# Optimization experiments

Hardware: AMD Instinct MI355X
Metric: run time of the kernel (lower is better)

## Reference

```python
import jax, jax.numpy as jnp
import numpy as np

N = 50000          # nodes
E = 500000         # edges (avg degree 10)
WIDTH = 128        # node feature width
HID = 128          # width * scale, scale=1 -> 2 heads of 64
HEAD = 64          # head_dim (module-level constant)
EMB = WIDTH // 2   # edge-embed width = 64
RES = 1.0
BOND = (5, 6, 2, 17)  # bond_size vocabularies


def setup_inputs() -> dict:
    key = jax.random.key(0)
    ks = jax.random.split(key, 24)
    w = lambda k, s: (jax.random.normal(k, s, jnp.float32) * 0.02)
    inp = {
        "x": jax.random.normal(ks[0], (N, WIDTH), jnp.float32),
        "edge_index": jax.random.randint(ks[1], (2, E), 0, N),
        "edge_attr": jax.random.randint(ks[2], (E, 4), 0, 3),
        # pre: Linear(width, width)
        "pre_w": w(ks[3], (WIDTH, WIDTH)), "pre_b": jnp.zeros((WIDTH,), jnp.float32),
        # msg[0..3]: Linear(width, hidden)
        "msg0_w": w(ks[4], (WIDTH, HID)), "msg0_b": jnp.zeros((HID,), jnp.float32),
        "msg1_w": w(ks[5], (WIDTH, HID)), "msg1_b": jnp.zeros((HID,), jnp.float32),
        "msg2_w": w(ks[6], (WIDTH, HID)), "msg2_b": jnp.zeros((HID,), jnp.float32),
        "msg3_w": w(ks[7], (WIDTH, HID)), "msg3_b": jnp.zeros((HID,), jnp.float32),
        # remix[0..2]: Linear(width//2, hidden)
        "remix0_w": w(ks[8], (EMB, HID)), "remix0_b": jnp.zeros((HID,), jnp.float32),
        "remix1_w": w(ks[9], (EMB, HID)), "remix1_b": jnp.zeros((HID,), jnp.float32),
        "remix2_w": w(ks[10], (EMB, HID)), "remix2_b": jnp.zeros((HID,), jnp.float32),
        # post: Linear(hidden, width)
        "post_w": w(ks[11], (HID, WIDTH)), "post_b": jnp.zeros((WIDTH,), jnp.float32),
        # EmbedBlock tables (bond_size + 1 rows each); tables 1..3 have padding_idx=0
        "emb0": w(ks[12], (BOND[0] + 1, EMB)),
        "emb1": w(ks[13], (BOND[1] + 1, EMB)).at[0].set(0.0),
        "emb2": w(ks[14], (BOND[2] + 1, EMB)).at[0].set(0.0),
        "emb3": w(ks[15], (BOND[3] + 1, EMB)).at[0].set(0.0),
        "einit": jnp.zeros((4,), jnp.float32),          # EmbedBlock.init0
        "init0": jnp.zeros((4,), jnp.float32),          # ConvBlock.init0 (hop*2+2)
    }
    return inp


def _gelu(v):
    return jax.nn.gelu(v, approximate=False)


def _ln(v):
    m = jnp.mean(v, axis=-1, keepdims=True)
    var = jnp.mean(jnp.square(v - m), axis=-1, keepdims=True)
    return (v - m) / jnp.sqrt(var + 1e-5)


def reference(x, edge_index, edge_attr, pre_w, pre_b, msg0_w, msg0_b,
              msg1_w, msg1_b, msg2_w, msg2_b, msg3_w, msg3_b,
              remix0_w, remix0_b, remix1_w, remix1_b, remix2_w, remix2_b,
              post_w, post_b, emb0, emb1, emb2, emb3, einit, init0):
    n = x.shape[0]
    e = edge_index.shape[1]
    xx = _ln(x @ pre_w + pre_b)  # pre: Linear + LayerNorm(no affine)
    # EmbedBlock: weighted sum of per-column embeddings, xw = exp(a)/sqrt(sum exp(a))
    xw = jnp.exp(einit) / jnp.sqrt(jnp.sum(jnp.exp(einit)))
    ee = (emb0[edge_attr[:, 0]] * xw[0] + emb1[edge_attr[:, 1]] * xw[1]
          + emb2[edge_attr[:, 2]] * xw[2] + emb3[edge_attr[:, 3]] * xw[3])  # [E, 64]
    src, dst = edge_index[0], edge_index[1]  # source_to_target: j=src, i=dst
    x_j = xx[src]
    x_i = xx[dst]
    scale_e = jnp.exp(init0[-2])
    scale_v = jnp.exp(init0[-1])
    q = x_i @ msg1_w + msg1_b + (ee @ remix0_w + remix0_b) * scale_e  # [E, HID]
    k = x_j @ msg2_w + msg2_b + (ee @ remix1_w + remix1_b) * scale_e
    v = _gelu(x_j @ msg3_w + msg3_b + (ee @ remix2_w + remix2_b) * scale_v)
    # per-head attention score, head_dim = 64
    att = jnp.sum((q * k).reshape(e, -1, HEAD), axis=-1, keepdims=True) / np.sqrt(HEAD)
    att = jnp.exp(att * init0[0] + init0[1])  # edge_type=0, hop=1
    msg = (v.reshape(e, -1, HEAD) * att).reshape(e, -1)  # [E, HID]
    agg = jax.ops.segment_sum(msg, dst, num_segments=n)  # scatter-add to targets
    xx = _gelu(xx @ msg0_w + msg0_b) + agg
    out = xx @ post_w + post_b
    return x + out * RES
```

## Files before the change

### kernel.cpp

```cpp
#include <hip/hip_runtime.h>
#include <cstdint>

#define WIDTH 128
#define NCOMBO 2268
#define XSL 136

typedef short bf16x8 __attribute__((ext_vector_type(8)));
typedef float f32x4  __attribute__((ext_vector_type(4)));

__device__ __forceinline__ float gelu_fast(float v) {
    float e = __expf(v * __builtin_fmaf(v * v, 0.0713548f, 1.5957691f));
    return v - v * __builtin_amdgcn_rcpf(e + 1.0f);
}
__device__ __forceinline__ short f2b(float f) {
    unsigned u = __float_as_uint(f);
    unsigned r = (u + 0x7FFFu + ((u >> 16) & 1u)) >> 16;
    return (short)r;
}
__device__ __forceinline__ float b2f(unsigned short s) {
    return __uint_as_float(((unsigned)s) << 16);
}
__device__ __forceinline__ float b2f_lo(unsigned u) { return __uint_as_float(u << 16); }
__device__ __forceinline__ float b2f_hi(unsigned u) { return __uint_as_float(u & 0xFFFF0000u); }
__device__ __forceinline__ unsigned pack2(float lo, float hi) {
    return (unsigned)(unsigned short)f2b(lo) | ((unsigned)(unsigned short)f2b(hi) << 16);
}

__global__ void k_prep(const float* __restrict__ einit, const float* __restrict__ init0,
                       const float* __restrict__ emb0, const float* __restrict__ emb1,
                       const float* __restrict__ emb2, const float* __restrict__ emb3,
                       const float* __restrict__ r0w, const float* __restrict__ r0b,
                       const float* __restrict__ r1w, const float* __restrict__ r1b,
                       const float* __restrict__ r2w, const float* __restrict__ r2b,
                       const float* __restrict__ pw0, const float* __restrict__ pw1,
                       const float* __restrict__ pw2, const float* __restrict__ pw3,
                       const float* __restrict__ pw4, const float* __restrict__ pw5,
                       short* __restrict__ o0, short* __restrict__ o1,
                       short* __restrict__ o2, short* __restrict__ o3,
                       short* __restrict__ o4, short* __restrict__ o5,
                       float* __restrict__ U, float* __restrict__ scal,
                       int* __restrict__ counts, int n) {
    int tid = blockIdx.x * blockDim.x + threadIdx.x;
    if (tid == 0) { scal[0] = init0[0]; scal[1] = init0[1]; }
    const int TOTW = 6 * 16384;
    const int TOTU = 3 * 34 * WIDTH;
    if (tid < TOTW) {
        int which = tid >> 14;
        int r = tid & 16383;
        int k = r >> 7, nn = r & 127;
        const float* w = (which == 0) ? pw0 : (which == 1) ? pw1 : (which == 2) ? pw2
                       : (which == 3) ? pw3 : (which == 4) ? pw4 : pw5;
        short* o = (which == 0) ? o0 : (which == 1) ? o1 : (which == 2) ? o2
                 : (which == 3) ? o3 : (which == 4) ? o4 : o5;
        o[nn * 128 + k] = f2b(w[k * 128 + nn]);
    } else if (tid < TOTW + TOTU) {
        int idx = tid - TOTW;
        float e0 = expf(einit[0]), e1 = expf(einit[1]), e2 = expf(einit[2]), e3 = expf(einit[3]);
        float inv = 1.0f / sqrtf(e0 + e1 + e2 + e3);
        float xw[4] = {e0 * inv, e1 * inv, e2 * inv, e3 * inv};
        float se = expf(init0[2]);
        float sv = expf(init0[3]);
        int r   = idx / (34 * WIDTH);
        int rem = idx - r * (34 * WIDTH);
        int g   = rem / WIDTH;
        int j   = rem - g * WIDTH;
        int cc, base;
        if (g >= 16)      { cc = 3; base = 16; }
        else if (g >= 13) { cc = 2; base = 13; }
        else if (g >= 6)  { cc = 1; base = 6; }
        else              { cc = 0; base = 0; }
        int i = g - base;
        const float* em = (cc == 0) ? emb0 : (cc == 1) ? emb1 : (cc == 2) ? emb2 : emb3;
        const float* w  = (r == 0) ? r0w : (r == 1) ? r1w : r2w;
        const float* rb = (r == 0) ? r0b : (r == 1) ? r1b : r2b;
        float s = (r == 2) ? sv : se;
        float acc = 0.0f;
        const float* erow = em + i * 64;
        for (int d = 0; d < 64; ++d) acc += erow[d] * w[d * WIDTH + j];
        float val = s * xw[cc] * acc;
        if (cc == 0) val += s * rb[j];
        U[idx] = val;
    } else if (tid < TOTW + TOTU + n) {
        counts[tid - TOTW - TOTU] = 0;
    }
}

__global__ void k_prepc(const float* __restrict__ U, const float* __restrict__ init0,
                        float* __restrict__ Uc) {
    int bi = blockIdx.x;
    int r  = bi / NCOMBO;
    if (r < 2 && init0[0] == 0.0f) return;
    int cb = bi - r * NCOMBO;
    int a  = cb / 378;
    int rm = cb - a * 378;
    int b  = rm / 54;
    rm -= b * 54;
    int c  = rm / 18;
    int d  = rm - c * 18;
    int j  = threadIdx.x;
    const float* Ur = U + r * 34 * WIDTH;
    Uc[(size_t)bi * WIDTH + j] = Ur[a * WIDTH + j] + Ur[(6 + b) * WIDTH + j]
                               + Ur[(13 + c) * WIDTH + j] + Ur[(16 + d) * WIDTH + j];
}

__global__ void k_hist(const int* __restrict__ edge_index, int* __restrict__ counts,
                       int* __restrict__ rank, int E) {
    int e = blockIdx.x * blockDim.x + threadIdx.x;
    if (e >= E) return;
    rank[e] = atomicAdd(&counts[edge_index[E + e]], 1);
}

__global__ void k_scan1(const int* __restrict__ counts, int* __restrict__ lscan,
                        int* __restrict__ partials, int n) {
    __shared__ int s[256];
    int t = threadIdx.x;
    int i = blockIdx.x * 256 + t;
    int v = (i < n) ? counts[i] : 0;
    s[t] = v;
    __syncthreads();
    for (int d = 1; d < 256; d <<= 1) {
        int u = (t >= d) ? s[t - d] : 0;
        __syncthreads();
        s[t] += u;
        __syncthreads();
    }
    if (i < n) lscan[i] = s[t];
    if (t == 255) partials[blockIdx.x] = s[255];
}

__global__ void k_scan2(int* __restrict__ partials, int nb,
                        int* __restrict__ offsets, int n) {
    __shared__ int s[1024];
    int t = threadIdx.x;
    int v = (t < nb) ? partials[t] : 0;
    s[t] = v;
    __syncthreads();
    for (int d = 1; d < 1024; d <<= 1) {
        int u = (t >= d) ? s[t - d] : 0;
        __syncthreads();
        s[t] += u;
        __syncthreads();
    }
    if (t < nb) partials[t] = s[t] - v;
    if (t == 1023) offsets[n] = s[1023];
}

__global__ void k_scan3(const int* __restrict__ counts, const int* __restrict__ lscan,
                        const int* __restrict__ partials, int* __restrict__ offsets, int n) {
    int i = blockIdx.x * 256 + threadIdx.x;
    if (i >= n) return;
    offsets[i] = partials[blockIdx.x] + lscan[i] - counts[i];
}

__global__ void k_scatter(const int* __restrict__ edge_index, const int* __restrict__ edge_attr,
                          const int* __restrict__ offsets, const int* __restrict__ rank,
                          unsigned* __restrict__ s_pk, int E) {
    int e = blockIdx.x * blockDim.x + threadIdx.x;
    if (e >= E) return;
    int src = edge_index[e];
    int dst = edge_index[E + e];
    int4 at = ((const int4*)edge_attr)[e];
    int combo = ((at.x * 7 + at.y) * 3 + at.z) * 18 + at.w;
    s_pk[offsets[dst] + rank[e]] = (unsigned)src | ((unsigned)combo << 17);
}

__global__ void __launch_bounds__(256, 2) k_gemm12(
        const float* __restrict__ x,
        const short* __restrict__ preT, const float* __restrict__ pre_b,
        const short* __restrict__ w0T, const float* __restrict__ b0,
        const short* __restrict__ w1T, const float* __restrict__ b1,
        const short* __restrict__ w2T, const float* __restrict__ b2,
        const short* __restrict__ w3T, const float* __restrict__ b3,
        const float* __restrict__ scal,
        short* __restrict__ Gb, float* __restrict__ A,
        short* __restrict__ Bb, short* __restrict__ Cb, int n) {
    __shared__ short xs[64 * XSL];
    int w    = threadIdx.x >> 6;
    int lane = threadIdx.x & 63;
    int quad = lane >> 4, l16 = lane & 15;
    int m0   = blockIdx.x * 64;

    bf16x8 Bg[2][4], Bc[2][4];
#pragma unroll
    for (int tt = 0; tt < 2; ++tt)
#pragma unroll
        for (int kc = 0; kc < 4; ++kc) {
            int row = (2 * w + tt) * 16 + l16;
            Bg[tt][kc] = *(const bf16x8*)(w0T + row * 128 + kc * 32 + quad * 8);
            Bc[tt][kc] = *(const bf16x8*)(w3T + row * 128 + kc * 32 + quad * 8);
        }

    {
        int mrow = m0 + w * 16;
        int mA = min(mrow + l16, n - 1);
        bf16x8 a[4];
#pragma unroll
        for (int kc = 0; kc < 4; ++kc) {
            const float* px = x + (size_t)mA * WIDTH + kc * 32 + quad * 8;
            float4 f0 = *(const float4*)(px);
            float4 f1 = *(const float4*)(px + 4);
            bf16x8 av;
            av[0] = f2b(f0.x); av[1] = f2b(f0.y); av[2] = f2b(f0.z); av[3] = f2b(f0.w);
            av[4] = f2b(f1.x); av[5] = f2b(f1.y); av[6] = f2b(f1.z); av[7] = f2b(f1.w);
            a[kc] = av;
        }
        f32x4 acc[8];
#pragma unroll
        for (int t = 0; t < 8; ++t) acc[t] = (f32x4){0.f, 0.f, 0.f, 0.f};
#pragma unroll
        for (int kc = 0; kc < 4; ++kc) {
#pragma unroll
            for (int t = 0; t < 8; ++t) {
                bf16x8 b = *(const bf16x8*)(preT + (t * 16 + l16) * 128 + kc * 32 + quad * 8);
                acc[t] = __builtin_amdgcn_mfma_f32_16x16x32_bf16(a[kc], b, acc[t], 0, 0, 0);
            }
        }
#pragma unroll
        for (int t = 0; t < 8; ++t) {
            float bv = pre_b[t * 16 + l16];
#pragma unroll
            for (int r = 0; r < 4; ++r) acc[t][r] += bv;
        }
#pragma unroll
        for (int r = 0; r < 4; ++r) {
            float s = 0.f, s2 = 0.f;
#pragma unroll
            for (int t = 0; t < 8; ++t) { float v = acc[t][r]; s += v; s2 += v * v; }
            s  += __shfl_xor(s, 1);  s2 += __shfl_xor(s2, 1);
            s  += __shfl_xor(s, 2);  s2 += __shfl_xor(s2, 2);
            s  += __shfl_xor(s, 4);  s2 += __shfl_xor(s2, 4);
            s  += __shfl_xor(s, 8);  s2 += __shfl_xor(s2, 8);
            float m   = s * (1.0f / WIDTH);
            float var = s2 * (1.0f / WIDTH) - m * m;
            float rs  = rsqrtf(var + 1e-5f);
#pragma unroll
            for (int t = 0; t < 8; ++t) acc[t][r] = (acc[t][r] - m) * rs;
        }
        int rowb = w * 16 + quad * 4;
#pragma unroll
        for (int t = 0; t < 8; ++t)
#pragma unroll
            for (int r = 0; r < 4; ++r)
                xs[(rowb + r) * XSL + t * 16 + l16] = f2b(acc[t][r]);
    }
    __syncthreads();

    bf16x8 a2[4][4];
#pragma unroll
    for (int i = 0; i < 4; ++i)
#pragma unroll
        for (int kc = 0; kc < 4; ++kc)
            a2[i][kc] = *(const bf16x8*)(&xs[(i * 16 + l16) * XSL + kc * 32 + quad * 8]);

    {
        f32x4 accG[4][2], accC[4][2];
#pragma unroll
        for (int i = 0; i < 4; ++i)
#pragma unroll
            for (int tt = 0; tt < 2; ++tt) {
                accG[i][tt] = (f32x4){0.f,0.f,0.f,0.f};
                accC[i][tt] = (f32x4){0.f,0.f,0.f,0.f};
            }
#pragma unroll
        for (int kc = 0; kc < 4; ++kc)
#pragma unroll
            for (int i = 0; i < 4; ++i)
#pragma unroll
                for (int tt = 0; tt < 2; ++tt) {
                    accG[i][tt] = __builtin_amdgcn_mfma_f32_16x16x32_bf16(a2[i][kc], Bg[tt][kc], accG[i][tt], 0, 0, 0);
                    accC[i][tt] = __builtin_amdgcn_mfma_f32_16x16x32_bf16(a2[i][kc], Bc[tt][kc], accC[i][tt], 0, 0, 0);
                }
#pragma unroll
        for (int tt = 0; tt < 2; ++tt) {
            int col = (2 * w + tt) * 16 + l16;
            float bg = b0[col];
            float bc = b3[col];
#pragma unroll
            for (int i = 0; i < 4; ++i)
#pragma unroll
                for (int r = 0; r < 4; ++r) {
                    int row = m0 + i * 16 + quad * 4 + r;
                    if (row < n) {
                        size_t idx = (size_t)row * WIDTH + col;
                        Gb[idx] = f2b(gelu_fast(accG[i][tt][r] + bg));
                        Cb[idx] = f2b(accC[i][tt][r] + bc);
                    }
                }
        }
    }
    if (scal[0] != 0.0f) {
        bf16x8 Ba[2][4], Bbf[2][4];
#pragma unroll
        for (int tt = 0; tt < 2; ++tt)
#pragma unroll
            for (int kc = 0; kc < 4; ++kc) {
                int row = (2 * w + tt) * 16 + l16;
                Ba[tt][kc]  = *(const bf16x8*)(w1T + row * 128 + kc * 32 + quad * 8);
                Bbf[tt][kc] = *(const bf16x8*)(w2T + row * 128 + kc * 32 + quad * 8);
            }
        f32x4 accA[4][2], accB[4][2];
#pragma unroll
        for (int i = 0; i < 4; ++i)
#pragma unroll
            for (int tt = 0; tt < 2; ++tt) {
                accA[i][tt] = (f32x4){0.f,0.f,0.f,0.f};
                accB[i][tt] = (f32x4){0.f,0.f,0.f,0.f};
            }
#pragma unroll
        for (int kc = 0; kc < 4; ++kc)
#pragma unroll
            for (int i = 0; i < 4; ++i)
#pragma unroll
                for (int tt = 0; tt < 2; ++tt) {
                    accA[i][tt] = __builtin_amdgcn_mfma_f32_16x16x32_bf16(a2[i][kc], Ba[tt][kc],  accA[i][tt], 0, 0, 0);
                    accB[i][tt] = __builtin_amdgcn_mfma_f32_16x16x32_bf16(a2[i][kc], Bbf[tt][kc], accB[i][tt], 0, 0, 0);
                }
#pragma unroll
        for (int tt = 0; tt < 2; ++tt) {
            int col = (2 * w + tt) * 16 + l16;
            float ba = b1[col];
            float bb = b2[col];
#pragma unroll
            for (int i = 0; i < 4; ++i)
#pragma unroll
                for (int r = 0; r < 4; ++r) {
                    int row = m0 + i * 16 + quad * 4 + r;
                    if (row < n) {
                        size_t idx = (size_t)row * WIDTH + col;
                        A[idx]  = accA[i][tt][r] + ba;
                        Bb[idx] = f2b(accB[i][tt][r] + bb);
                    }
                }
        }
    }
}

__global__ void __launch_bounds__(256)
k_agg(const int* __restrict__ offsets, const unsigned* __restrict__ s_pk,
      const float* __restrict__ A, const short* __restrict__ Bb,
      const short* __restrict__ Cb, const float* __restrict__ Uc,
      const float* __restrict__ scal, const short* __restrict__ Gb,
      short* __restrict__ hb, int n) {
    int wid = threadIdx.x >> 6;
    int L   = threadIdx.x & 63;
    int node = blockIdx.x * 4 + wid;
    if (node >= n) return;
    int start = offsets[node];
    int end   = offsets[node + 1];

    const unsigned* Cb32 = (const unsigned*)Cb;
    const unsigned* Bb32 = (const unsigned*)Bb;
    const float2* U0c2 = (const float2*)(Uc);
    const float2* U1c2 = (const float2*)(Uc + (size_t)NCOMBO * WIDTH);
    const float2* U2c2 = (const float2*)(Uc + 2 * (size_t)NCOMBO * WIDTH);

    float i0 = scal[0], i1 = scal[1];
    float acc0 = 0.0f, acc1 = 0.0f;

    if (i0 == 0.0f) {
        int p = start;
        for (; p + 2 <= end; p += 2) {
            unsigned pk0 = s_pk[p], pk1 = s_pk[p + 1];
            unsigned sA = pk0 & 0x1FFFFu, cA = pk0 >> 17;
            unsigned sB = pk1 & 0x1FFFFu, cB = pk1 >> 17;
            unsigned cc0 = Cb32[sA * 64 + L];
            float2   uu0 = U2c2[cA * 64 + L];
            unsigned cc1 = Cb32[sB * 64 + L];
            float2   uu1 = U2c2[cB * 64 + L];
            acc0 += gelu_fast(b2f_lo(cc0) + uu0.x);
            acc1 += gelu_fast(b2f_hi(cc0) + uu0.y);
            acc0 += gelu_fast(b2f_lo(cc1) + uu1.x);
            acc1 += gelu_fast(b2f_hi(cc1) + uu1.y);
        }
        if (p < end) {
            unsigned pk0 = s_pk[p];
            unsigned sA = pk0 & 0x1FFFFu, cA = pk0 >> 17;
            unsigned cc0 = Cb32[sA * 64 + L];
            float2   uu0 = U2c2[cA * 64 + L];
            acc0 += gelu_fast(b2f_lo(cc0) + uu0.x);
            acc1 += gelu_fast(b2f_hi(cc0) + uu0.y);
        }
        float s = __expf(i1);
        acc0 *= s; acc1 *= s;
    } else {
        float2 av = *(const float2*)(A + (size_t)node * WIDTH + 2 * L);
        for (int p = start; p < end; ++p) {
            unsigned pk = s_pk[p];
            unsigned sA = pk & 0x1FFFFu, cA = pk >> 17;
            float2 u0 = U0c2[cA * 64 + L];
            float2 u1 = U1c2[cA * 64 + L];
            float2 u2 = U2c2[cA * 64 + L];
            unsigned bb = Bb32[sA * 64 + L];
            unsigned cc = Cb32[sA * 64 + L];
            float q0 = av.x + u0.x, q1 = av.y + u0.y;
            float k0 = b2f_lo(bb) + u1.x, k1 = b2f_hi(bb) + u1.y;
            float v0 = gelu_fast(b2f_lo(cc) + u2.x);
            float v1 = gelu_fast(b2f_hi(cc) + u2.y);
            float s = q0 * k0 + q1 * k1;
            s += __shfl_xor(s, 1);
            s += __shfl_xor(s, 2);
            s += __shfl_xor(s, 4);
            s += __shfl_xor(s, 8);
            s += __shfl_xor(s, 16);
            float att = __expf(s * 0.125f * i0 + i1);
            acc0 += v0 * att;
            acc1 += v1 * att;
        }
    }
    unsigned g = ((const unsigned*)Gb)[(size_t)node * 64 + L];
    ((unsigned*)hb)[(size_t)node * 64 + L] = pack2(b2f_lo(g) + acc0, b2f_hi(g) + acc1);
}

__global__ void __launch_bounds__(256, 2) k_post(
        const float* __restrict__ x, const short* __restrict__ hb,
        const short* __restrict__ postT, const float* __restrict__ post_b,
        float* __restrict__ out, int n) {
    int w    = threadIdx.x >> 6;
    int lane = threadIdx.x & 63;
    int quad = lane >> 4, l16 = lane & 15;
    int m0   = blockIdx.x * 64;

    bf16x8 Bp[2][4];
#pragma unroll
    for (int tt = 0; tt < 2; ++tt)
#pragma unroll
        for (int kc = 0; kc < 4; ++kc) {
            int row = (2 * w + tt) * 16 + l16;
            Bp[tt][kc] = *(const bf16x8*)(postT + row * 128 + kc * 32 + quad * 8);
        }

    bf16x8 a[4][4];
#pragma unroll
    for (int i = 0; i < 4; ++i) {
        int mA = min(m0 + i * 16 + l16, n - 1);
#pragma unroll
        for (int kc = 0; kc < 4; ++kc)
            a[i][kc] = *(const bf16x8*)(hb + (size_t)mA * WIDTH + kc * 32 + quad * 8);
    }

    f32x4 acc[4][2];
#pragma unroll
    for (int i = 0; i < 4; ++i)
#pragma unroll
        for (int tt = 0; tt < 2; ++tt) acc[i][tt] = (f32x4){0.f,0.f,0.f,0.f};
#pragma unroll
    for (int kc = 0; kc < 4; ++kc)
#pragma unroll
        for (int i = 0; i < 4; ++i)
#pragma unroll
            for (int tt = 0; tt < 2; ++tt)
                acc[i][tt] = __builtin_amdgcn_mfma_f32_16x16x32_bf16(a[i][kc], Bp[tt][kc], acc[i][tt], 0, 0, 0);

#pragma unroll
    for (int tt = 0; tt < 2; ++tt) {
        int col = (2 * w + tt) * 16 + l16;
        float bv = post_b[col];
#pragma unroll
        for (int i = 0; i < 4; ++i)
#pragma unroll
            for (int r = 0; r < 4; ++r) {
                int row = m0 + i * 16 + quad * 4 + r;
                if (row < n) {
                    size_t idx = (size_t)row * WIDTH + col;
                    out[idx] = x[idx] + acc[i][tt][r] + bv;
                }
            }
    }
}

extern "C" void kernel_launch(void* const* d_in, const int* in_sizes, int n_in,
                              void* d_out, int out_size, void* d_ws, size_t ws_size,
                              hipStream_t stream) {
    const float* x      = (const float*)d_in[0];
    const int*   eidx   = (const int*)d_in[1];
    const int*   eattr  = (const int*)d_in[2];
    const float* pre_w  = (const float*)d_in[3];
    const float* pre_b  = (const float*)d_in[4];
    const float* msg0_w = (const float*)d_in[5];
    const float* msg0_b = (const float*)d_in[6];
    const float* msg1_w = (const float*)d_in[7];
    const float* msg1_b = (const float*)d_in[8];
    const float* msg2_w = (const float*)d_in[9];
    const float* msg2_b = (const float*)d_in[10];
    const float* msg3_w = (const float*)d_in[11];
    const float* msg3_b = (const float*)d_in[12];
    const float* r0w    = (const float*)d_in[13];
    const float* r0b    = (const float*)d_in[14];
    const float* r1w    = (const float*)d_in[15];
    const float* r1b    = (const float*)d_in[16];
    const float* r2w    = (const float*)d_in[17];
    const float* r2b    = (const float*)d_in[18];
    const float* post_w = (const float*)d_in[19];
    const float* post_b = (const float*)d_in[20];
    const float* emb0   = (const float*)d_in[21];
    const float* emb1   = (const float*)d_in[22];
    const float* emb2   = (const float*)d_in[23];
    const float* emb3   = (const float*)d_in[24];
    const float* einit  = (const float*)d_in[25];
    const float* init0  = (const float*)d_in[26];

    int n = in_sizes[0] / WIDTH;
    int E = in_sizes[2] / 4;
    size_t NW = (size_t)n * WIDTH;

    float* ws   = (float*)d_ws;
    float* A    = ws;
    float* U    = ws + NW;
    float* Uc   = U + 3 * 34 * WIDTH;
    float* scal = Uc + 3 * (size_t)NCOMBO * WIDTH;
    short* sw   = (short*)(scal + 2);
    short* preT  = sw;
    short* w0T   = sw + 16384;
    short* w1T   = sw + 2 * 16384;
    short* w2T   = sw + 3 * 16384;
    short* w3T   = sw + 4 * 16384;
    short* postT = sw + 5 * 16384;
    short* Bb    = sw + 6 * 16384;
    short* Cb    = Bb + NW;
    short* Gb    = Cb + NW;
    short* hb    = Gb + NW;
    int*      ib       = (int*)(hb + NW);
    int*      offsets  = ib;
    int*      counts   = offsets + (n + 1);
    int*      lscan    = counts + n;
    int*      partials = lscan + n;
    int*      rank     = partials + 1024;
    unsigned* s_pk     = (unsigned*)(rank + E);

    int prep_total = 6 * 16384 + 3 * 34 * WIDTH + n;
    k_prep<<<(prep_total + 255) / 256, 256, 0, stream>>>(
        einit, init0, emb0, emb1, emb2, emb3,
        r0w, r0b, r1w, r1b, r2w, r2b,
        pre_w, msg0_w, msg1_w, msg2_w, msg3_w, post_w,
        preT, w0T, w1T, w2T, w3T, postT, U, scal, counts, n);
    k_prepc<<<3 * NCOMBO, 128, 0, stream>>>(U, init0, Uc);

    int eb = (E + 255) / 256;
    k_hist<<<eb, 256, 0, stream>>>(eidx, counts, rank, E);
    int sb = (n + 255) / 256;
    k_scan1<<<sb, 256, 0, stream>>>(counts, lscan, partials, n);
    k_scan2<<<1, 1024, 0, stream>>>(partials, sb, offsets, n);
    k_scan3<<<sb, 256, 0, stream>>>(counts, lscan, partials, offsets, n);
    k_scatter<<<eb, 256, 0, stream>>>(eidx, eattr, offsets, rank, s_pk, E);

    int gb = (n + 63) / 64;
    k_gemm12<<<gb, 256, 0, stream>>>(x, preT, pre_b, w0T, msg0_b, w1T, msg1_b,
                                     w2T, msg2_b, w3T, msg3_b, scal, Gb, A, Bb, Cb, n);
    k_agg<<<(n + 3) / 4, 256, 0, stream>>>(offsets, s_pk, A, Bb, Cb, Uc, scal, Gb, hb, n);
    k_post<<<gb, 256, 0, stream>>>(x, hb, postT, post_b, (float*)d_out, n);
}
```

Before: 280.3 us.

## Pre-swizzle weights into MFMA fragment order and stage GEMM I/O through LDS

Weights are now stored in the exact per-lane MFMA fragment order, so each wave's B-operand loads become contiguous 16-byte reads. In k_gemm12 and k_post, the x/hb input tiles are loaded cooperatively with coalesced vector loads into LDS, and the Gb/Cb and out tiles are written back through LDS as full-row vector stores. This replaces strided per-element global accesses. The cost is more shared memory per block, which may lower occupancy, and extra __syncthreads barriers.

```diff
diff --git a/kernel.cpp b/kernel.cpp
--- a/kernel.cpp
+++ b/kernel.cpp
@@ -4,6 +4,7 @@
 #define WIDTH 128
 #define NCOMBO 2268
 #define XSL 136
+#define OSL 132
 
 typedef short bf16x8 __attribute__((ext_vector_type(8)));
 typedef float f32x4  __attribute__((ext_vector_type(4)));
@@ -16,9 +17,6 @@
     unsigned u = __float_as_uint(f);
     unsigned r = (u + 0x7FFFu + ((u >> 16) & 1u)) >> 16;
     return (short)r;
-}
-__device__ __forceinline__ float b2f(unsigned short s) {
-    return __uint_as_float(((unsigned)s) << 16);
 }
 __device__ __forceinline__ float b2f_lo(unsigned u) { return __uint_as_float(u << 16); }
 __device__ __forceinline__ float b2f_hi(unsigned u) { return __uint_as_float(u & 0xFFFF0000u); }
@@ -47,12 +45,17 @@
     if (tid < TOTW) {
         int which = tid >> 14;
         int r = tid & 16383;
-        int k = r >> 7, nn = r & 127;
+        int t    = r >> 11;
+        int kc   = (r >> 9) & 3;
+        int lane = (r >> 3) & 63;
+        int j    = r & 7;
+        int k  = kc * 32 + ((lane >> 4) << 3) + j;
+        int nn = (t << 4) + (lane & 15);
         const float* w = (which == 0) ? pw0 : (which == 1) ? pw1 : (which == 2) ? pw2
                        : (which == 3) ? pw3 : (which == 4) ? pw4 : pw5;
         short* o = (which == 0) ? o0 : (which == 1) ? o1 : (which == 2) ? o2
                  : (which == 3) ? o3 : (which == 4) ? o4 : o5;
-        o[nn * 128 + k] = f2b(w[k * 128 + nn]);
+        o[r] = f2b(w[k * 128 + nn]);
     } else if (tid < TOTW + TOTU) {
         int idx = tid - TOTW;
         float e0 = expf(einit[0]), e1 = expf(einit[1]), e2 = expf(einit[2]), e3 = expf(einit[3]);
@@ -166,17 +169,19 @@
 
 __global__ void __launch_bounds__(256, 2) k_gemm12(
         const float* __restrict__ x,
-        const short* __restrict__ preT, const float* __restrict__ pre_b,
-        const short* __restrict__ w0T, const float* __restrict__ b0,
-        const short* __restrict__ w1T, const float* __restrict__ b1,
-        const short* __restrict__ w2T, const float* __restrict__ b2,
-        const short* __restrict__ w3T, const float* __restrict__ b3,
+        const short* __restrict__ preF, const float* __restrict__ pre_b,
+        const short* __restrict__ w0F, const float* __restrict__ b0,
+        const short* __restrict__ w1F, const float* __restrict__ b1,
+        const short* __restrict__ w2F, const float* __restrict__ b2,
+        const short* __restrict__ w3F, const float* __restrict__ b3,
         const float* __restrict__ scal,
         short* __restrict__ Gb, float* __restrict__ A,
         short* __restrict__ Bb, short* __restrict__ Cb, int n) {
-    __shared__ short xs[64 * XSL];
-    int w    = threadIdx.x >> 6;
-    int lane = threadIdx.x & 63;
+    __shared__ short xs_raw[64 * XSL];
+    __shared__ short xs_xx[64 * XSL];
+    int tid  = threadIdx.x;
+    int w    = tid >> 6;
+    int lane = tid & 63;
     int quad = lane >> 4, l16 = lane & 15;
     int m0   = blockIdx.x * 64;
 
@@ -185,36 +190,39 @@
     for (int tt = 0; tt < 2; ++tt)
 #pragma unroll
         for (int kc = 0; kc < 4; ++kc) {
-            int row = (2 * w + tt) * 16 + l16;
-            Bg[tt][kc] = *(const bf16x8*)(w0T + row * 128 + kc * 32 + quad * 8);
-            Bc[tt][kc] = *(const bf16x8*)(w3T + row * 128 + kc * 32 + quad * 8);
-        }
+            int fo = (((2 * w + tt) * 4 + kc) * 64 + lane) * 8;
+            Bg[tt][kc] = *(const bf16x8*)(w0F + fo);
+            Bc[tt][kc] = *(const bf16x8*)(w3F + fo);
+        }
+
+#pragma unroll
+    for (int it = 0; it < 8; ++it) {
+        int fi  = it * 256 + tid;
+        int row = fi >> 5, c4 = fi & 31;
+        int gr  = min(m0 + row, n - 1);
+        float4 v = ((const float4*)x)[(size_t)gr * 32 + c4];
+        uint2 p;
+        p.x = pack2(v.x, v.y);
+        p.y = pack2(v.z, v.w);
+        *(uint2*)(&xs_raw[row * XSL + c4 * 4]) = p;
+    }
+    __syncthreads();
 
     {
-        int mrow = m0 + w * 16;
-        int mA = min(mrow + l16, n - 1);
         bf16x8 a[4];
 #pragma unroll
-        for (int kc = 0; kc < 4; ++kc) {
-            const float* px = x + (size_t)mA * WIDTH + kc * 32 + quad * 8;
-            float4 f0 = *(const float4*)(px);
-            float4 f1 = *(const float4*)(px + 4);
-            bf16x8 av;
-            av[0] = f2b(f0.x); av[1] = f2b(f0.y); av[2] = f2b(f0.z); av[3] = f2b(f0.w);
-            av[4] = f2b(f1.x); av[5] = f2b(f1.y); av[6] = f2b(f1.z); av[7] = f2b(f1.w);
-            a[kc] = av;
-        }
+        for (int kc = 0; kc < 4; ++kc)
+            a[kc] = *(const bf16x8*)(&xs_raw[(w * 16 + l16) * XSL + kc * 32 + quad * 8]);
         f32x4 acc[8];
 #pragma unroll
         for (int t = 0; t < 8; ++t) acc[t] = (f32x4){0.f, 0.f, 0.f, 0.f};
 #pragma unroll
-        for (int kc = 0; kc < 4; ++kc) {
+        for (int kc = 0; kc < 4; ++kc)
 #pragma unroll
             for (int t = 0; t < 8; ++t) {
-                bf16x8 b = *(const bf16x8*)(preT + (t * 16 + l16) * 128 + kc * 32 + quad * 8);
+                bf16x8 b = *(const bf16x8*)(preF + ((t * 4 + kc) * 64 + lane) * 8);
                 acc[t] = __builtin_amdgcn_mfma_f32_16x16x32_bf16(a[kc], b, acc[t], 0, 0, 0);
             }
-        }
 #pragma unroll
         for (int t = 0; t < 8; ++t) {
             float bv = pre_b[t * 16 + l16];
@@ -241,7 +249,7 @@
         for (int t = 0; t < 8; ++t)
 #pragma unroll
             for (int r = 0; r < 4; ++r)
-                xs[(rowb + r) * XSL + t * 16 + l16] = f2b(acc[t][r]);
+                xs_xx[(rowb + r) * XSL + t * 16 + l16] = f2b(acc[t][r]);
     }
     __syncthreads();
 
@@ -250,7 +258,8 @@
     for (int i = 0; i < 4; ++i)
 #pragma unroll
         for (int kc = 0; kc < 4; ++kc)
-            a2[i][kc] = *(const bf16x8*)(&xs[(i * 16 + l16) * XSL + kc * 32 + quad * 8]);
+            a2[i][kc] = *(const bf16x8*)(&xs_xx[(i * 16 + l16) * XSL + kc * 32 + quad * 8]);
+    __syncthreads();
 
     {
         f32x4 accG[4][2], accC[4][2];
@@ -279,24 +288,33 @@
             for (int i = 0; i < 4; ++i)
 #pragma unroll
                 for (int r = 0; r < 4; ++r) {
-                    int row = m0 + i * 16 + quad * 4 + r;
-                    if (row < n) {
-                        size_t idx = (size_t)row * WIDTH + col;
-                        Gb[idx] = f2b(gelu_fast(accG[i][tt][r] + bg));
-                        Cb[idx] = f2b(accC[i][tt][r] + bc);
-                    }
+                    int row = i * 16 + quad * 4 + r;
+                    xs_raw[row * XSL + col] = f2b(gelu_fast(accG[i][tt][r] + bg));
+                    xs_xx[row * XSL + col]  = f2b(accC[i][tt][r] + bc);
                 }
         }
     }
+    __syncthreads();
+
+#pragma unroll
+    for (int it = 0; it < 4; ++it) {
+        int si  = it * 256 + tid;
+        int row = si >> 4, c8 = si & 15;
+        if (m0 + row < n) {
+            *(bf16x8*)(Gb + (size_t)(m0 + row) * WIDTH + c8 * 8) = *(const bf16x8*)(&xs_raw[row * XSL + c8 * 8]);
+            *(bf16x8*)(Cb + (size_t)(m0 + row) * WIDTH + c8 * 8) = *(const bf16x8*)(&xs_xx[row * XSL + c8 * 8]);
+        }
+    }
+
     if (scal[0] != 0.0f) {
         bf16x8 Ba[2][4], Bbf[2][4];
 #pragma unroll
         for (int tt = 0; tt < 2; ++tt)
 #pragma unroll
             for (int kc = 0; kc < 4; ++kc) {
-                int row = (2 * w + tt) * 16 + l16;
-                Ba[tt][kc]  = *(const bf16x8*)(w1T + row * 128 + kc * 32 + quad * 8);
-                Bbf[tt][kc] = *(const bf16x8*)(w2T + row * 128 + kc * 32 + quad * 8);
+                int fo = (((2 * w + tt) * 4 + kc) * 64 + lane) * 8;
+                Ba[tt][kc]  = *(const bf16x8*)(w1F + fo);
+                Bbf[tt][kc] = *(const bf16x8*)(w2F + fo);
             }
         f32x4 accA[4][2], accB[4][2];
 #pragma unroll
@@ -413,10 +431,13 @@
 
 __global__ void __launch_bounds__(256, 2) k_post(
         const float* __restrict__ x, const short* __restrict__ hb,
-        const short* __restrict__ postT, const float* __restrict__ post_b,
+        const short* __restrict__ postF, const float* __restrict__ post_b,
         float* __restrict__ out, int n) {
-    int w    = threadIdx.x >> 6;
-    int lane = threadIdx.x & 63;
+    __shared__ short hs[64 * XSL];
+    __shared__ float os[64 * OSL];
+    int tid  = threadIdx.x;
+    int w    = tid >> 6;
+    int lane = tid & 63;
     int quad = lane >> 4, l16 = lane & 15;
     int m0   = blockIdx.x * 64;
 
@@ -424,19 +445,24 @@
 #pragma unroll
     for (int tt = 0; tt < 2; ++tt)
 #pragma unroll
-        for (int kc = 0; kc < 4; ++kc) {
-            int row = (2 * w + tt) * 16 + l16;
-            Bp[tt][kc] = *(const bf16x8*)(postT + row * 128 + kc * 32 + quad * 8);
-        }
+        for (int kc = 0; kc < 4; ++kc)
+            Bp[tt][kc] = *(const bf16x8*)(postF + (((2 * w + tt) * 4 + kc) * 64 + lane) * 8);
+
+#pragma unroll
+    for (int it = 0; it < 4; ++it) {
+        int si  = it * 256 + tid;
+        int row = si >> 4, c8 = si & 15;
+        int gr  = min(m0 + row, n - 1);
+        *(bf16x8*)(&hs[row * XSL + c8 * 8]) = *(const bf16x8*)(hb + (size_t)gr * WIDTH + c8 * 8);
+    }
+    __syncthreads();
 
     bf16x8 a[4][4];
 #pragma unroll
-    for (int i = 0; i < 4; ++i) {
-        int mA = min(m0 + i * 16 + l16, n - 1);
-#pragma unroll
-        for (int kc = 0; kc < 4; ++kc)
-            a[i][kc] = *(const bf16x8*)(hb + (size_t)mA * WIDTH + kc * 32 + quad * 8);
-    }
+    for (int i = 0; i < 4; ++i)
+#pragma unroll
+        for (int kc = 0; kc < 4; ++kc)
+            a[i][kc] = *(const bf16x8*)(&hs[(i * 16 + l16) * XSL + kc * 32 + quad * 8]);
 
     f32x4 acc[4][2];
 #pragma unroll
@@ -458,13 +484,21 @@
 #pragma unroll
         for (int i = 0; i < 4; ++i)
 #pragma unroll
-            for (int r = 0; r < 4; ++r) {
-                int row = m0 + i * 16 + quad * 4 + r;
-                if (row < n) {
-                    size_t idx = (size_t)row * WIDTH + col;
-                    out[idx] = x[idx] + acc[i][tt][r] + bv;
-                }
-            }
+            for (int r = 0; r < 4; ++r)
+                os[(i * 16 + quad * 4 + r) * OSL + col] = acc[i][tt][r] + bv;
+    }
+    __syncthreads();
+
+#pragma unroll
+    for (int it = 0; it < 8; ++it) {
+        int fi  = it * 256 + tid;
+        int row = fi >> 5, c4 = fi & 31;
+        if (m0 + row < n) {
+            float4 xv = ((const float4*)x)[(size_t)(m0 + row) * 32 + c4];
+            float4 av = *(const float4*)(&os[row * OSL + c4 * 4]);
+            float4 ov = {xv.x + av.x, xv.y + av.y, xv.z + av.z, xv.w + av.w};
+            ((float4*)out)[(size_t)(m0 + row) * 32 + c4] = ov;
+        }
     }
 }
 
@@ -509,12 +543,12 @@
     float* Uc   = U + 3 * 34 * WIDTH;
     float* scal = Uc + 3 * (size_t)NCOMBO * WIDTH;
     short* sw   = (short*)(scal + 2);
-    short* preT  = sw;
-    short* w0T   = sw + 16384;
-    short* w1T   = sw + 2 * 16384;
-    short* w2T   = sw + 3 * 16384;
-    short* w3T   = sw + 4 * 16384;
-    short* postT = sw + 5 * 16384;
+    short* preF  = sw;
+    short* w0F   = sw + 16384;
+    short* w1F   = sw + 2 * 16384;
+    short* w2F   = sw + 3 * 16384;
+    short* w3F   = sw + 4 * 16384;
+    short* postF = sw + 5 * 16384;
     short* Bb    = sw + 6 * 16384;
     short* Cb    = Bb + NW;
     short* Gb    = Cb + NW;
@@ -532,7 +566,7 @@
         einit, init0, emb0, emb1, emb2, emb3,
         r0w, r0b, r1w, r1b, r2w, r2b,
         pre_w, msg0_w, msg1_w, msg2_w, msg3_w, post_w,
-        preT, w0T, w1T, w2T, w3T, postT, U, scal, counts, n);
+        preF, w0F, w1F, w2F, w3F, postF, U, scal, counts, n);
     k_prepc<<<3 * NCOMBO, 128, 0, stream>>>(U, init0, Uc);
 
     int eb = (E + 255) / 256;
@@ -544,8 +578,8 @@
     k_scatter<<<eb, 256, 0, stream>>>(eidx, eattr, offsets, rank, s_pk, E);
 
     int gb = (n + 63) / 64;
-    k_gemm12<<<gb, 256, 0, stream>>>(x, preT, pre_b, w0T, msg0_b, w1T, msg1_b,
-                                     w2T, msg2_b, w3T, msg3_b, scal, Gb, A, Bb, Cb, n);
+    k_gemm12<<<gb, 256, 0, stream>>>(x, preF, pre_b, w0F, msg0_b, w1F, msg1_b,
+                                     w2F, msg2_b, w3F, msg3_b, scal, Gb, A, Bb, Cb, n);
     k_agg<<<(n + 3) / 4, 256, 0, stream>>>(offsets, s_pk, A, Bb, Cb, Uc, scal, Gb, hb, n);
-    k_post<<<gb, 256, 0, stream>>>(x, hb, postT, post_b, (float*)d_out, n);
-}
+    k_post<<<gb, 256, 0, stream>>>(x, hb, postF, post_b, (float*)d_out, n);
+}
```

Result: faster. 247.5 us (-11.7%).
